# Performance work log

Hardware: AMD Instinct MI355X
Metric: run time of the kernel (lower is better)

## Reference

```python
import jax, jax.numpy as jnp
import numpy as np

VOCAB, EMBED, HIDDEN, OUT = 32000, 512, 1024, 32000
BATCH, SEQ = 8, 256


def setup_inputs() -> dict:
    key = jax.random.key(0)
    ks = jax.random.split(key, 8)
    s_e = 1.0 / np.sqrt(EMBED)
    s_h = 1.0 / np.sqrt(HIDDEN)
    return {
        "inputs": jax.random.randint(ks[0], (BATCH, SEQ), 0, VOCAB, dtype=jnp.int64),
        "embed_table": jax.random.normal(ks[1], (VOCAB, EMBED), dtype=jnp.float32),
        "W_ih": jax.random.uniform(ks[2], (HIDDEN, EMBED), jnp.float32, -s_h, s_h),
        "W_hh": jax.random.uniform(ks[3], (HIDDEN, HIDDEN), jnp.float32, -s_h, s_h),
        "b_ih": jax.random.uniform(ks[4], (HIDDEN,), jnp.float32, -s_h, s_h),
        "b_hh": jax.random.uniform(ks[5], (HIDDEN,), jnp.float32, -s_h, s_h),
        "W_fc": jax.random.uniform(ks[6], (OUT, HIDDEN), jnp.float32, -s_h, s_h),
        "b_fc": jax.random.uniform(ks[7], (OUT,), jnp.float32, -s_h, s_h),
    }


def reference(inputs, embed_table, W_ih, W_hh, b_ih, b_hh, W_fc, b_fc):
    # embeds: [B, T, E] -> [T, B, E] for scan over time
    embeds = embed_table[inputs]
    x_t = jnp.transpose(embeds, (1, 0, 2))
    # precompute input contribution for all steps: [T, B, H]
    xproj = jnp.einsum("tbe,he->tbh", x_t, W_ih) + b_ih

    def step(h, xp):
        h_new = jnp.tanh(xp + h @ W_hh.T + b_hh)
        return h_new, h_new

    h0 = jnp.zeros((inputs.shape[0], W_hh.shape[0]), dtype=embeds.dtype)
    _, hs = jax.lax.scan(step, h0, xproj)  # hs: [T, B, H]
    # fc projection per step: [T, B, OUT] -> [B, T, OUT]
    logits = jnp.einsum("tbh,oh->tbo", hs, W_fc) + b_fc
    return jnp.transpose(logits, (1, 0, 2))
```

## Files before the change

### kernel.cpp

```cpp
#include <hip/hip_runtime.h>
#include <stdint.h>

#define T_SEQ 256
#define NB    8
#define EMB   512
#define HID   1024
#define NOUT  32000
#define RING  16
#define SEN   0x40004000u

typedef float    f32x4  __attribute__((ext_vector_type(4)));
typedef unsigned int u32x4 __attribute__((ext_vector_type(4)));
typedef __bf16   bf16x8 __attribute__((ext_vector_type(8)));

#define AS1 __attribute__((address_space(1)))
#define AS3 __attribute__((address_space(3)))

__device__ __forceinline__ uint32_t f2bf(float f) {
    uint32_t u = __builtin_bit_cast(uint32_t, f);
    u += 0x7FFFu + ((u >> 16) & 1u);
    return (u >> 16);
}

__device__ __forceinline__ bf16x8 mk_hi(u32x4 a, u32x4 b) {
    u32x4 r;
    r.x = __builtin_amdgcn_perm(a.y, a.x, 0x07060302u);
    r.y = __builtin_amdgcn_perm(a.w, a.z, 0x07060302u);
    r.z = __builtin_amdgcn_perm(b.y, b.x, 0x07060302u);
    r.w = __builtin_amdgcn_perm(b.w, b.z, 0x07060302u);
    return __builtin_bit_cast(bf16x8, r);
}
__device__ __forceinline__ bf16x8 mk_lo(u32x4 a, u32x4 b) {
    u32x4 r;
    r.x = __builtin_amdgcn_perm(a.y, a.x, 0x05040100u);
    r.y = __builtin_amdgcn_perm(a.w, a.z, 0x05040100u);
    r.z = __builtin_amdgcn_perm(b.y, b.x, 0x05040100u);
    r.w = __builtin_amdgcn_perm(b.w, b.z, 0x05040100u);
    return __builtin_bit_cast(bf16x8, r);
}

__global__ void k_fill(unsigned int* __restrict__ p) {
    int i = blockIdx.x * blockDim.x + threadIdx.x;
    unsigned int* a = p + (size_t)i * 4;
#pragma unroll
    for (int j = 0; j < 4; ++j)
        (void)__hip_atomic_exchange(a + j, SEN, __ATOMIC_RELAXED, __HIP_MEMORY_SCOPE_AGENT);
}

__global__ void k_convert_wfc(const float* __restrict__ src, unsigned short* __restrict__ dst) {
    int i = blockIdx.x * blockDim.x + threadIdx.x;
    const f32x4* s4 = (const f32x4*)src;
    int n4 = NOUT * HID / 4;
    int stride = gridDim.x * blockDim.x;
    for (int idx = i; idx < n4; idx += stride) {
        f32x4 v = s4[idx];
        uint2 o;
        o.x = f2bf(v.x) | (f2bf(v.y) << 16);
        o.y = f2bf(v.z) | (f2bf(v.w) << 16);
        ((uint2*)dst)[idx] = o;
    }
}

__global__ __launch_bounds__(256) void k_xproj(
        const int* __restrict__ inputs, const float* __restrict__ embed,
        const float* __restrict__ W_ih, const float* __restrict__ b_ih,
        float* __restrict__ xproj) {
    __shared__ float As[64][33];
    __shared__ float Bs[64][33];
    __shared__ int   idx_s[64];
    const int tid = threadIdx.x;
    const int bm = blockIdx.y, bn = blockIdx.x;
    if (tid < 64) {
        int m = bm * 64 + tid;
        idx_s[tid] = inputs[(m & 7) * T_SEQ + (m >> 3)];
    }
    __syncthreads();
    const int ty = tid >> 4, tx = tid & 15;
    const int lr = tid >> 2, lc = (tid & 3) * 8;
    float acc[4][4] = {};
    for (int kk = 0; kk < EMB; kk += 32) {
        __syncthreads();
        const float* arow = embed + (size_t)idx_s[lr] * EMB + kk + lc;
        f32x4 a0 = *(const f32x4*)arow;
        f32x4 a1 = *(const f32x4*)(arow + 4);
        const float* brow = W_ih + (size_t)(bn * 64 + lr) * EMB + kk + lc;
        f32x4 b0 = *(const f32x4*)brow;
        f32x4 b1 = *(const f32x4*)(brow + 4);
#pragma unroll
        for (int u = 0; u < 4; ++u) {
            As[lr][lc + u] = a0[u]; As[lr][lc + 4 + u] = a1[u];
            Bs[lr][lc + u] = b0[u]; Bs[lr][lc + 4 + u] = b1[u];
        }
        __syncthreads();
#pragma unroll
        for (int k = 0; k < 32; ++k) {
            float av[4], bv[4];
#pragma unroll
            for (int i = 0; i < 4; ++i) av[i] = As[ty * 4 + i][k];
#pragma unroll
            for (int j = 0; j < 4; ++j) bv[j] = Bs[tx * 4 + j][k];
#pragma unroll
            for (int i = 0; i < 4; ++i)
#pragma unroll
                for (int j = 0; j < 4; ++j) acc[i][j] += av[i] * bv[j];
        }
    }
#pragma unroll
    for (int i = 0; i < 4; ++i) {
        int m = bm * 64 + ty * 4 + i;
#pragma unroll
        for (int j = 0; j < 4; ++j) {
            int n = bn * 64 + tx * 4 + j;
            xproj[(size_t)m * HID + n] = acc[i][j] + b_ih[n];
        }
    }
}

#define DO_CHUNK(qa, qb, WH, WL, ACC) do {                                      \
    bf16x8 ah = mk_hi(qa, qb);                                                  \
    bf16x8 al = mk_lo(qa, qb);                                                  \
    ACC = __builtin_amdgcn_mfma_f32_16x16x32_bf16(ah, WH, ACC, 0, 0, 0);        \
    ACC = __builtin_amdgcn_mfma_f32_16x16x32_bf16(al, WH, ACC, 0, 0, 0);        \
    ACC = __builtin_amdgcn_mfma_f32_16x16x32_bf16(ah, WL, ACC, 0, 0, 0);        \
} while (0)

__global__ __launch_bounds__(256, 1) void k_rnn(
        const float* __restrict__ W_hh, const float* __restrict__ b_hh,
        const float* __restrict__ xproj,
        unsigned int* __restrict__ hpk ,
        unsigned short* __restrict__ hs ) {
    __shared__ __align__(16) unsigned int hlds[1024];
    __shared__ float part[2][4][16];
    const int tid = threadIdx.x;
    const int w   = tid >> 6;
    const int ln  = tid & 63;
    const int blk = blockIdx.x;
    const int chain  = blk >> 5;
    const int member = blk & 31;
    const int cg = w & 1;
    const int kh = w >> 1;
    const int col0 = member * 32 + cg * 16;
    unsigned int* ring = hpk + (size_t)chain * (RING * 1024);

    const float* wrow = W_hh + (size_t)(col0 + (ln & 15)) * HID;
    bf16x8 whi[16], wlo[16];
#pragma unroll
    for (int cc = 0; cc < 16; ++cc) {
        int k0 = kh * 512 + cc * 32 + (ln >> 4) * 8;
        f32x4 wa = *(const f32x4*)(wrow + k0);
        f32x4 wb = *(const f32x4*)(wrow + k0 + 4);
        float wv[8] = { wa.x, wa.y, wa.z, wa.w, wb.x, wb.y, wb.z, wb.w };
        uint32_t hu[8], lu[8];
#pragma unroll
        for (int j = 0; j < 8; ++j) {
            hu[j] = f2bf(wv[j]);
            float hif = __builtin_bit_cast(float, hu[j] << 16);
            lu[j] = f2bf(wv[j] - hif);
        }
        u32x4 ph = { hu[0] | (hu[1] << 16), hu[2] | (hu[3] << 16),
                     hu[4] | (hu[5] << 16), hu[6] | (hu[7] << 16) };
        u32x4 pl = { lu[0] | (lu[1] << 16), lu[2] | (lu[3] << 16),
                     lu[4] | (lu[5] << 16), lu[6] | (lu[7] << 16) };
        whi[cc] = __builtin_bit_cast(bf16x8, ph);
        wlo[cc] = __builtin_bit_cast(bf16x8, pl);
    }
    const float bhh = (ln < 16) ? b_hh[col0 + ln] : 0.f;

    for (int t = 0; t < T_SEQ; ++t) {
        float xp = 0.f;
        if (kh == 0 && ln < 16)
            xp = xproj[(size_t)(t * NB + chain) * HID + col0 + ln];

        if (t > 0) {
            const unsigned int* hp = ring + (size_t)((t - 1) & (RING - 1)) * 1024
                                          + w * 256 + ln * 4;
            u32x4 q;
            do {
                asm volatile("global_load_dwordx4 %0, %1, off sc0 sc1\n\t"
                             "s_waitcnt vmcnt(0)"
                             : "=&v"(q) : "v"(hp) : "memory");
            } while (q.x == SEN || q.y == SEN || q.z == SEN || q.w == SEN);
            *(u32x4*)&hlds[w * 256 + ln * 4] = q;
        }
        __syncthreads();

        f32x4 acc0 = {0.f, 0.f, 0.f, 0.f}, acc1 = {0.f, 0.f, 0.f, 0.f};
        if (t > 0) {
            const int lsub = (ln >> 4) * 8;
#pragma unroll
            for (int cc = 0; cc < 16; ++cc) {
                int ab = kh * 512 + cc * 32 + lsub;
                u32x4 qa = *(const u32x4*)&hlds[ab];
                u32x4 qb = *(const u32x4*)&hlds[ab + 4];
                if (cc & 1) { DO_CHUNK(qa, qb, whi[cc], wlo[cc], acc1); }
                else        { DO_CHUNK(qa, qb, whi[cc], wlo[cc], acc0); }
            }
        }
        if (ln < 16) part[t & 1][w][ln] = acc0.x + acc1.x;
        __syncthreads();

        if (kh == 0 && ln < 16) {
            float sum = part[t & 1][w][ln] + part[t & 1][w + 2][ln];
            int colp = col0 + ln;
            float x = xp + sum + bhh;
            float h = tanhf(x);
            uint32_t hi = f2bf(h);
            float hif = __builtin_bit_cast(float, hi << 16);
            uint32_t lo = f2bf(h - hif);
            uint32_t pk = (hi << 16) | lo;
            (void)__hip_atomic_exchange(ring + (size_t)(t & (RING - 1)) * 1024 + colp,
                                        pk, __ATOMIC_RELAXED, __HIP_MEMORY_SCOPE_AGENT);
            (void)__hip_atomic_exchange(ring + (size_t)((t + RING - 3) & (RING - 1)) * 1024 + colp,
                                        SEN, __ATOMIC_RELAXED, __HIP_MEMORY_SCOPE_AGENT);
            hs[(size_t)(t * NB + chain) * HID + colp] = (unsigned short)hi;
        }
    }
}

__global__ void k_fc(const unsigned short* __restrict__ A,
                     const unsigned short* __restrict__ Bw,
                     const float* __restrict__ bias,
                     float* __restrict__ out) {
    __shared__ __align__(16) unsigned short As[128 * 32];
    __shared__ __align__(16) unsigned short Bs[128 * 32];
    const int tid = threadIdx.x;
    const int w = tid >> 6, ln = tid & 63;
    const int bm = blockIdx.x, bn = blockIdx.y;
    const int wm = (w >> 1) * 64, wn = (w & 1) * 64;
    const int srow = tid >> 2;
    const int scol = (tid & 3) * 8;
    const unsigned short* Ag = A  + (size_t)(bm * 128 + srow) * 1024 + scol;
    const unsigned short* Bg = Bw + (size_t)(bn * 128 + srow) * 1024 + scol;
    unsigned short* ldsA0 = As + w * 512;
    unsigned short* ldsA1 = As + 2048 + w * 512;
    unsigned short* ldsB0 = Bs + w * 512;
    unsigned short* ldsB1 = Bs + 2048 + w * 512;

    f32x4 acc[4][4] = {};
    const int fr = ln & 15;
    const int kq = (ln >> 4) * 8;

    for (int kk = 0; kk < 1024; kk += 32) {
        __syncthreads();
        __builtin_amdgcn_global_load_lds((const AS1 void*)(Ag + kk),             (AS3 void*)ldsA0, 16, 0, 0);
        __builtin_amdgcn_global_load_lds((const AS1 void*)(Ag + 64 * 1024 + kk), (AS3 void*)ldsA1, 16, 0, 0);
        __builtin_amdgcn_global_load_lds((const AS1 void*)(Bg + kk),             (AS3 void*)ldsB0, 16, 0, 0);
        __builtin_amdgcn_global_load_lds((const AS1 void*)(Bg + 64 * 1024 + kk), (AS3 void*)ldsB1, 16, 0, 0);
        __syncthreads();
        bf16x8 af[4], bf[4];
#pragma unroll
        for (int i = 0; i < 4; ++i)
            af[i] = *(const bf16x8*)&As[(wm + i * 16 + fr) * 32 + kq];
#pragma unroll
        for (int j = 0; j < 4; ++j)
            bf[j] = *(const bf16x8*)&Bs[(wn + j * 16 + fr) * 32 + kq];
#pragma unroll
        for (int i = 0; i < 4; ++i)
#pragma unroll
            for (int j = 0; j < 4; ++j)
                acc[i][j] = __builtin_amdgcn_mfma_f32_16x16x32_bf16(af[i], bf[j], acc[i][j], 0, 0, 0);
    }

    const int fq = ln >> 4;
#pragma unroll
    for (int i = 0; i < 4; ++i) {
#pragma unroll
        for (int j = 0; j < 4; ++j) {
            int n = bn * 128 + wn + j * 16 + fr;
            float bv = bias[n];
#pragma unroll
            for (int r = 0; r < 4; ++r) {
                int m = bm * 128 + wm + i * 16 + fq * 4 + r;
                int t = m >> 3, b = m & 7;
                out[(size_t)b * T_SEQ * NOUT + (size_t)t * NOUT + n] = acc[i][j][r] + bv;
            }
        }
    }
}

extern "C" void kernel_launch(void* const* d_in, const int* in_sizes, int n_in,
                              void* d_out, int out_size, void* d_ws, size_t ws_size,
                              hipStream_t stream) {
    const int*   inputs = (const int*)d_in[0];
    const float* embed  = (const float*)d_in[1];
    const float* W_ih   = (const float*)d_in[2];
    const float* W_hh   = (const float*)d_in[3];
    const float* b_ih   = (const float*)d_in[4];
    const float* b_hh   = (const float*)d_in[5];
    const float* W_fc   = (const float*)d_in[6];
    const float* b_fc   = (const float*)d_in[7];
    float* out = (float*)d_out;

    char* ws = (char*)d_ws;
    unsigned int*   hpk   = (unsigned int*)(ws);
    float*          xproj = (float*)(ws + 524288);
    unsigned short* hs    = (unsigned short*)(ws + 524288 + 8388608);
    unsigned short* wfcb  = (unsigned short*)(ws + 524288 + 8388608 + 4194304);

    k_fill<<<128, 256, 0, stream>>>(hpk);
    k_convert_wfc<<<2048, 256, 0, stream>>>(W_fc, wfcb);
    k_xproj<<<dim3(16, 32), 256, 0, stream>>>(inputs, embed, W_ih, b_ih, xproj);
    k_rnn<<<256, 256, 0, stream>>>(W_hh, b_hh, xproj, hpk, hs);
    k_fc<<<dim3(16, 250), 256, 0, stream>>>(hs, wfcb, b_fc, out);
}
```

Baseline: 811.8 us.

## Fuse RNN recurrence and FC GEMM into one persistent kernel with progress counters

Merges the recurrent kernel and the output projection GEMM into a single launch. The first 256 blocks run the RNN and bump per-chain progress counters as timesteps complete. The remaining 256 blocks grab FC column strips via an atomic ticket and spin-wait until the needed rows of hidden states are published before computing each 128-row tile. This lets the large FC GEMM overlap with the latency-bound sequential recurrence, at the cost of spin polling, co-residency assumptions (launch bounds raised to 2 blocks/CU), and FC blocks sharing CUs with the RNN blocks.

```diff
diff --git a/kernel.cpp b/kernel.cpp
--- a/kernel.cpp
+++ b/kernel.cpp
@@ -8,6 +8,7 @@
 #define NOUT  32000
 #define RING  16
 #define SEN   0x40004000u
+#define NSTRIP 250
 
 typedef float    f32x4  __attribute__((ext_vector_type(4)));
 typedef unsigned int u32x4 __attribute__((ext_vector_type(4)));
@@ -124,156 +125,197 @@
     ACC = __builtin_amdgcn_mfma_f32_16x16x32_bf16(ah, WL, ACC, 0, 0, 0);        \
 } while (0)
 
-__global__ __launch_bounds__(256, 1) void k_rnn(
+__global__ __launch_bounds__(256, 2) void k_mega(
         const float* __restrict__ W_hh, const float* __restrict__ b_hh,
         const float* __restrict__ xproj,
         unsigned int* __restrict__ hpk ,
-        unsigned short* __restrict__ hs ) {
-    __shared__ __align__(16) unsigned int hlds[1024];
-    __shared__ float part[2][4][16];
+        unsigned short* __restrict__ hs ,
+        const unsigned short* __restrict__ wfcb ,
+        const float* __restrict__ b_fc,
+        float* __restrict__ out,
+        unsigned int* __restrict__ chaincnt ,
+        unsigned int* __restrict__ ticket) {
+    __shared__ __align__(16) char smem[16896];
     const int tid = threadIdx.x;
     const int w   = tid >> 6;
     const int ln  = tid & 63;
     const int blk = blockIdx.x;
-    const int chain  = blk >> 5;
-    const int member = blk & 31;
-    const int cg = w & 1;
-    const int kh = w >> 1;
-    const int col0 = member * 32 + cg * 16;
-    unsigned int* ring = hpk + (size_t)chain * (RING * 1024);
-
-    const float* wrow = W_hh + (size_t)(col0 + (ln & 15)) * HID;
-    bf16x8 whi[16], wlo[16];
-#pragma unroll
-    for (int cc = 0; cc < 16; ++cc) {
-        int k0 = kh * 512 + cc * 32 + (ln >> 4) * 8;
-        f32x4 wa = *(const f32x4*)(wrow + k0);
-        f32x4 wb = *(const f32x4*)(wrow + k0 + 4);
-        float wv[8] = { wa.x, wa.y, wa.z, wa.w, wb.x, wb.y, wb.z, wb.w };
-        uint32_t hu[8], lu[8];
-#pragma unroll
-        for (int j = 0; j < 8; ++j) {
-            hu[j] = f2bf(wv[j]);
-            float hif = __builtin_bit_cast(float, hu[j] << 16);
-            lu[j] = f2bf(wv[j] - hif);
-        }
-        u32x4 ph = { hu[0] | (hu[1] << 16), hu[2] | (hu[3] << 16),
-                     hu[4] | (hu[5] << 16), hu[6] | (hu[7] << 16) };
-        u32x4 pl = { lu[0] | (lu[1] << 16), lu[2] | (lu[3] << 16),
-                     lu[4] | (lu[5] << 16), lu[6] | (lu[7] << 16) };
-        whi[cc] = __builtin_bit_cast(bf16x8, ph);
-        wlo[cc] = __builtin_bit_cast(bf16x8, pl);
-    }
-    const float bhh = (ln < 16) ? b_hh[col0 + ln] : 0.f;
-
-    for (int t = 0; t < T_SEQ; ++t) {
-        float xp = 0.f;
-        if (kh == 0 && ln < 16)
-            xp = xproj[(size_t)(t * NB + chain) * HID + col0 + ln];
-
-        if (t > 0) {
-            const unsigned int* hp = ring + (size_t)((t - 1) & (RING - 1)) * 1024
-                                          + w * 256 + ln * 4;
-            u32x4 q;
-            do {
-                asm volatile("global_load_dwordx4 %0, %1, off sc0 sc1\n\t"
-                             "s_waitcnt vmcnt(0)"
-                             : "=&v"(q) : "v"(hp) : "memory");
-            } while (q.x == SEN || q.y == SEN || q.z == SEN || q.w == SEN);
-            *(u32x4*)&hlds[w * 256 + ln * 4] = q;
-        }
-        __syncthreads();
-
-        f32x4 acc0 = {0.f, 0.f, 0.f, 0.f}, acc1 = {0.f, 0.f, 0.f, 0.f};
-        if (t > 0) {
-            const int lsub = (ln >> 4) * 8;
-#pragma unroll
-            for (int cc = 0; cc < 16; ++cc) {
-                int ab = kh * 512 + cc * 32 + lsub;
-                u32x4 qa = *(const u32x4*)&hlds[ab];
-                u32x4 qb = *(const u32x4*)&hlds[ab + 4];
-                if (cc & 1) { DO_CHUNK(qa, qb, whi[cc], wlo[cc], acc1); }
-                else        { DO_CHUNK(qa, qb, whi[cc], wlo[cc], acc0); }
-            }
-        }
-        if (ln < 16) part[t & 1][w][ln] = acc0.x + acc1.x;
-        __syncthreads();
-
-        if (kh == 0 && ln < 16) {
-            float sum = part[t & 1][w][ln] + part[t & 1][w + 2][ln];
-            int colp = col0 + ln;
-            float x = xp + sum + bhh;
-            float h = tanhf(x);
-            uint32_t hi = f2bf(h);
-            float hif = __builtin_bit_cast(float, hi << 16);
-            uint32_t lo = f2bf(h - hif);
-            uint32_t pk = (hi << 16) | lo;
-            (void)__hip_atomic_exchange(ring + (size_t)(t & (RING - 1)) * 1024 + colp,
-                                        pk, __ATOMIC_RELAXED, __HIP_MEMORY_SCOPE_AGENT);
-            (void)__hip_atomic_exchange(ring + (size_t)((t + RING - 3) & (RING - 1)) * 1024 + colp,
-                                        SEN, __ATOMIC_RELAXED, __HIP_MEMORY_SCOPE_AGENT);
-            hs[(size_t)(t * NB + chain) * HID + colp] = (unsigned short)hi;
-        }
-    }
-}
-
-__global__ void k_fc(const unsigned short* __restrict__ A,
-                     const unsigned short* __restrict__ Bw,
-                     const float* __restrict__ bias,
-                     float* __restrict__ out) {
-    __shared__ __align__(16) unsigned short As[128 * 32];
-    __shared__ __align__(16) unsigned short Bs[128 * 32];
-    const int tid = threadIdx.x;
-    const int w = tid >> 6, ln = tid & 63;
-    const int bm = blockIdx.x, bn = blockIdx.y;
+
+    if (blk < 256) {
+        unsigned int* hlds = (unsigned int*)smem;
+        float (*part)[4][16] = (float (*)[4][16])(smem + 4096);
+        const int chain  = blk >> 5;
+        const int member = blk & 31;
+        const int cg = w & 1;
+        const int kh = w >> 1;
+        const int col0 = member * 32 + cg * 16;
+        unsigned int* ring = hpk + (size_t)chain * (RING * 1024);
+        unsigned int* cc_p = chaincnt + chain * 32;
+
+        const float* wrow = W_hh + (size_t)(col0 + (ln & 15)) * HID;
+        bf16x8 whi[16], wlo[16];
+#pragma unroll
+        for (int cc = 0; cc < 16; ++cc) {
+            int k0 = kh * 512 + cc * 32 + (ln >> 4) * 8;
+            f32x4 wa = *(const f32x4*)(wrow + k0);
+            f32x4 wb = *(const f32x4*)(wrow + k0 + 4);
+            float wv[8] = { wa.x, wa.y, wa.z, wa.w, wb.x, wb.y, wb.z, wb.w };
+            uint32_t hu[8], lu[8];
+#pragma unroll
+            for (int j = 0; j < 8; ++j) {
+                hu[j] = f2bf(wv[j]);
+                float hif = __builtin_bit_cast(float, hu[j] << 16);
+                lu[j] = f2bf(wv[j] - hif);
+            }
+            u32x4 ph = { hu[0] | (hu[1] << 16), hu[2] | (hu[3] << 16),
+                         hu[4] | (hu[5] << 16), hu[6] | (hu[7] << 16) };
+            u32x4 pl = { lu[0] | (lu[1] << 16), lu[2] | (lu[3] << 16),
+                         lu[4] | (lu[5] << 16), lu[6] | (lu[7] << 16) };
+            whi[cc] = __builtin_bit_cast(bf16x8, ph);
+            wlo[cc] = __builtin_bit_cast(bf16x8, pl);
+        }
+        const float bhh = (ln < 16) ? b_hh[col0 + ln] : 0.f;
+
+        for (int t = 0; t < T_SEQ; ++t) {
+            float xp = 0.f;
+            if (kh == 0 && ln < 16)
+                xp = xproj[(size_t)(t * NB + chain) * HID + col0 + ln];
+
+            if (t > 0) {
+                const unsigned int* hp = ring + (size_t)((t - 1) & (RING - 1)) * 1024
+                                              + w * 256 + ln * 4;
+                u32x4 q;
+                do {
+                    asm volatile("global_load_dwordx4 %0, %1, off sc0 sc1\n\t"
+                                 "s_waitcnt vmcnt(0)"
+                                 : "=&v"(q) : "v"(hp) : "memory");
+                } while (q.x == SEN || q.y == SEN || q.z == SEN || q.w == SEN);
+                *(u32x4*)&hlds[w * 256 + ln * 4] = q;
+            }
+            __syncthreads();
+            if (t > 0 && tid == 0)
+                (void)__hip_atomic_fetch_add(cc_p, 1u,
+                                             __ATOMIC_RELAXED, __HIP_MEMORY_SCOPE_AGENT);
+
+            f32x4 acc0 = {0.f, 0.f, 0.f, 0.f}, acc1 = {0.f, 0.f, 0.f, 0.f};
+            if (t > 0) {
+                const int lsub = (ln >> 4) * 8;
+#pragma unroll
+                for (int cc = 0; cc < 16; ++cc) {
+                    int ab = kh * 512 + cc * 32 + lsub;
+                    u32x4 qa = *(const u32x4*)&hlds[ab];
+                    u32x4 qb = *(const u32x4*)&hlds[ab + 4];
+                    if (cc & 1) { DO_CHUNK(qa, qb, whi[cc], wlo[cc], acc1); }
+                    else        { DO_CHUNK(qa, qb, whi[cc], wlo[cc], acc0); }
+                }
+            }
+            if (ln < 16) part[t & 1][w][ln] = acc0.x + acc1.x;
+            __syncthreads();
+
+            if (kh == 0 && ln < 16) {
+                float sum = part[t & 1][w][ln] + part[t & 1][w + 2][ln];
+                int colp = col0 + ln;
+                float x = xp + sum + bhh;
+                float h = tanhf(x);
+                uint32_t hi = f2bf(h);
+                float hif = __builtin_bit_cast(float, hi << 16);
+                uint32_t lo = f2bf(h - hif);
+                uint32_t pk = (hi << 16) | lo;
+                (void)__hip_atomic_exchange(ring + (size_t)(t & (RING - 1)) * 1024 + colp,
+                                            pk, __ATOMIC_RELAXED, __HIP_MEMORY_SCOPE_AGENT);
+                (void)__hip_atomic_exchange(ring + (size_t)((t + RING - 3) & (RING - 1)) * 1024 + colp,
+                                            SEN, __ATOMIC_RELAXED, __HIP_MEMORY_SCOPE_AGENT);
+                unsigned short* aa = hs + (size_t)(t * NB + chain) * HID + colp;
+                asm volatile("global_store_short %0, %1, off sc0 sc1"
+                             :: "v"(aa), "v"(hi) : "memory");
+            }
+        }
+        asm volatile("s_waitcnt vmcnt(0)" ::: "memory");
+        __syncthreads();
+        if (tid == 0)
+            (void)__hip_atomic_fetch_add(cc_p, 1u,
+                                         __ATOMIC_RELAXED, __HIP_MEMORY_SCOPE_AGENT);
+        return;
+    }
+
+    unsigned short* As = (unsigned short*)smem;
+    unsigned short* Bs = (unsigned short*)(smem + 8192);
+    int* ticket_s = (int*)(smem + 16384);
     const int wm = (w >> 1) * 64, wn = (w & 1) * 64;
+    const int fr = ln & 15;
+    const int kq = (ln >> 4) * 8;
     const int srow = tid >> 2;
     const int scol = (tid & 3) * 8;
-    const unsigned short* Ag = A  + (size_t)(bm * 128 + srow) * 1024 + scol;
-    const unsigned short* Bg = Bw + (size_t)(bn * 128 + srow) * 1024 + scol;
-    unsigned short* ldsA0 = As + w * 512;
-    unsigned short* ldsA1 = As + 2048 + w * 512;
-    unsigned short* ldsB0 = Bs + w * 512;
-    unsigned short* ldsB1 = Bs + 2048 + w * 512;
-
-    f32x4 acc[4][4] = {};
-    const int fr = ln & 15;
-    const int kq = (ln >> 4) * 8;
-
-    for (int kk = 0; kk < 1024; kk += 32) {
-        __syncthreads();
-        __builtin_amdgcn_global_load_lds((const AS1 void*)(Ag + kk),             (AS3 void*)ldsA0, 16, 0, 0);
-        __builtin_amdgcn_global_load_lds((const AS1 void*)(Ag + 64 * 1024 + kk), (AS3 void*)ldsA1, 16, 0, 0);
-        __builtin_amdgcn_global_load_lds((const AS1 void*)(Bg + kk),             (AS3 void*)ldsB0, 16, 0, 0);
-        __builtin_amdgcn_global_load_lds((const AS1 void*)(Bg + 64 * 1024 + kk), (AS3 void*)ldsB1, 16, 0, 0);
-        __syncthreads();
-        bf16x8 af[4], bf[4];
-#pragma unroll
-        for (int i = 0; i < 4; ++i)
-            af[i] = *(const bf16x8*)&As[(wm + i * 16 + fr) * 32 + kq];
-#pragma unroll
-        for (int j = 0; j < 4; ++j)
-            bf[j] = *(const bf16x8*)&Bs[(wn + j * 16 + fr) * 32 + kq];
-#pragma unroll
-        for (int i = 0; i < 4; ++i)
-#pragma unroll
-            for (int j = 0; j < 4; ++j)
-                acc[i][j] = __builtin_amdgcn_mfma_f32_16x16x32_bf16(af[i], bf[j], acc[i][j], 0, 0, 0);
-    }
-
-    const int fq = ln >> 4;
-#pragma unroll
-    for (int i = 0; i < 4; ++i) {
-#pragma unroll
-        for (int j = 0; j < 4; ++j) {
-            int n = bn * 128 + wn + j * 16 + fr;
-            float bv = bias[n];
-#pragma unroll
-            for (int r = 0; r < 4; ++r) {
-                int m = bm * 128 + wm + i * 16 + fq * 4 + r;
-                int t = m >> 3, b = m & 7;
-                out[(size_t)b * T_SEQ * NOUT + (size_t)t * NOUT + n] = acc[i][j][r] + bv;
-            }
+
+    for (;;) {
+        __syncthreads();
+        if (tid == 0) *ticket_s = (int)atomicAdd(ticket, 1u);
+        __syncthreads();
+        int bn = *ticket_s;
+        if (bn >= NSTRIP) break;
+
+        const unsigned short* Bg = wfcb + (size_t)(bn * 128 + srow) * 1024 + scol;
+
+        for (int bm = 0; bm < 16; ++bm) {
+            if (w == 0) {
+                unsigned int thr = 512u * (unsigned int)(bm + 1);
+                const unsigned int* cp = chaincnt + (ln & 7) * 32;
+                for (;;) {
+                    unsigned int v;
+                    asm volatile("global_load_dword %0, %1, off sc0 sc1\n\t"
+                                 "s_waitcnt vmcnt(0)"
+                                 : "=v"(v) : "v"(cp) : "memory");
+                    bool ok = (ln < 8) ? (v >= thr) : true;
+                    if (__all(ok)) break;
+                    __builtin_amdgcn_s_sleep(16);
+                }
+            }
+            __syncthreads();
+
+            const unsigned short* Ag = hs + (size_t)(bm * 128 + srow) * 1024 + scol;
+            unsigned short* ldsA0 = As + w * 512;
+            unsigned short* ldsA1 = As + 2048 + w * 512;
+            unsigned short* ldsB0 = Bs + w * 512;
+            unsigned short* ldsB1 = Bs + 2048 + w * 512;
+
+            f32x4 acc[4][4] = {};
+            for (int kk = 0; kk < 1024; kk += 32) {
+                __syncthreads();
+                __builtin_amdgcn_global_load_lds((const AS1 void*)(Ag + kk),             (AS3 void*)ldsA0, 16, 0, 0);
+                __builtin_amdgcn_global_load_lds((const AS1 void*)(Ag + 64 * 1024 + kk), (AS3 void*)ldsA1, 16, 0, 0);
+                __builtin_amdgcn_global_load_lds((const AS1 void*)(Bg + kk),             (AS3 void*)ldsB0, 16, 0, 0);
+                __builtin_amdgcn_global_load_lds((const AS1 void*)(Bg + 64 * 1024 + kk), (AS3 void*)ldsB1, 16, 0, 0);
+                __syncthreads();
+                bf16x8 af[4], bfj[4];
+#pragma unroll
+                for (int i = 0; i < 4; ++i)
+                    af[i] = *(const bf16x8*)&As[(wm + i * 16 + fr) * 32 + kq];
+#pragma unroll
+                for (int j = 0; j < 4; ++j)
+                    bfj[j] = *(const bf16x8*)&Bs[(wn + j * 16 + fr) * 32 + kq];
+#pragma unroll
+                for (int i = 0; i < 4; ++i)
+#pragma unroll
+                    for (int j = 0; j < 4; ++j)
+                        acc[i][j] = __builtin_amdgcn_mfma_f32_16x16x32_bf16(af[i], bfj[j], acc[i][j], 0, 0, 0);
+            }
+
+            const int fq = ln >> 4;
+#pragma unroll
+            for (int i = 0; i < 4; ++i) {
+#pragma unroll
+                for (int j = 0; j < 4; ++j) {
+                    int n = bn * 128 + wn + j * 16 + fr;
+                    float bv = b_fc[n];
+#pragma unroll
+                    for (int r = 0; r < 4; ++r) {
+                        int m = bm * 128 + wm + i * 16 + fq * 4 + r;
+                        int t = m >> 3, b = m & 7;
+                        out[(size_t)b * T_SEQ * NOUT + (size_t)t * NOUT + n] = acc[i][j][r] + bv;
+                    }
+                }
+            }
+            __syncthreads();
         }
     }
 }
@@ -292,14 +334,17 @@
     float* out = (float*)d_out;
 
     char* ws = (char*)d_ws;
-    unsigned int*   hpk   = (unsigned int*)(ws);
-    float*          xproj = (float*)(ws + 524288);
-    unsigned short* hs    = (unsigned short*)(ws + 524288 + 8388608);
-    unsigned short* wfcb  = (unsigned short*)(ws + 524288 + 8388608 + 4194304);
-
+    unsigned int*   chaincnt = (unsigned int*)(ws);
+    unsigned int*   ticket   = (unsigned int*)(ws + 2048);
+    unsigned int*   hpk      = (unsigned int*)(ws + 4096);
+    float*          xproj    = (float*)(ws + 4096 + 524288);
+    unsigned short* hs       = (unsigned short*)(ws + 4096 + 524288 + 8388608);
+    unsigned short* wfcb     = (unsigned short*)(ws + 4096 + 524288 + 8388608 + 4194304);
+
+    hipMemsetAsync(ws, 0, 4096, stream);
     k_fill<<<128, 256, 0, stream>>>(hpk);
     k_convert_wfc<<<2048, 256, 0, stream>>>(W_fc, wfcb);
     k_xproj<<<dim3(16, 32), 256, 0, stream>>>(inputs, embed, W_ih, b_ih, xproj);
-    k_rnn<<<256, 256, 0, stream>>>(W_hh, b_hh, xproj, hpk, hs);
-    k_fc<<<dim3(16, 250), 256, 0, stream>>>(hs, wfcb, b_fc, out);
-}
+    k_mega<<<512, 256, 0, stream>>>(W_hh, b_hh, xproj, hpk, hs,
+                                    wfcb, b_fc, out, chaincnt, ticket);
+}
```

Result: slower. 1.130 ms (+39.2%).
